# Optimization experiments

Hardware: AMD Instinct MI355X
Metric: run time of the kernel (lower is better)

The kernel has to match this reference:

```python
import jax, jax.numpy as jnp
import numpy as np

B, T, D, H = 1024, 128, 128, 8
HS = D // H  # 16, matches the hard-coded 16**-0.5 scale
EPS = 1e-5


def setup_inputs() -> dict:
    key = jax.random.key(0)
    ks = jax.random.split(key, 12)
    s = 0.02
    return {
        "x": jax.random.normal(ks[0], (B, T, D), jnp.float32),
        "Wq": jax.random.normal(ks[1], (H, D, HS), jnp.float32) * s,
        "Wk": jax.random.normal(ks[2], (H, D, HS), jnp.float32) * s,
        "Wv": jax.random.normal(ks[3], (H, D, HS), jnp.float32) * s,
        "Wo": jax.random.normal(ks[4], (D, D), jnp.float32) * s,
        "bo": jnp.zeros((D,), jnp.float32),
        "W1": jax.random.normal(ks[5], (D, 4 * D), jnp.float32) * s,
        "b1": jnp.zeros((4 * D,), jnp.float32),
        "W2": jax.random.normal(ks[6], (4 * D, D), jnp.float32) * s,
        "b2": jnp.zeros((D,), jnp.float32),
        "g1": jnp.ones((D,), jnp.float32),
        "be1": jnp.zeros((D,), jnp.float32),
        "g2": jnp.ones((D,), jnp.float32),
        "be2": jnp.zeros((D,), jnp.float32),
    }


def _layernorm(x, g, b):
    mu = jnp.mean(x, axis=-1, keepdims=True)
    var = jnp.mean(jnp.square(x - mu), axis=-1, keepdims=True)
    return (x - mu) * jax.lax.rsqrt(var + EPS) * g + b


def _block(x, Wq, Wk, Wv, Wo, bo, W1, b1, W2, b2, g1, be1, g2, be2):
    h = _layernorm(x, g1, be1)
    q = jnp.einsum('btd,hde->bhte', h, Wq)
    k = jnp.einsum('btd,hde->bhte', h, Wk)
    v = jnp.einsum('btd,hde->bhte', h, Wv)
    scores = jnp.einsum('bhte,bhse->bhts', q, k) * (16.0 ** -0.5)
    causal = jnp.tril(jnp.ones((T, T), bool))
    scores = jnp.where(causal, scores, -jnp.inf)
    wei = jax.nn.softmax(scores, axis=-1)  # dropout off (eval)
    o = jnp.einsum('bhts,bhse->bhte', wei, v)
    o = jnp.transpose(o, (0, 2, 1, 3)).reshape(x.shape[0], T, D)  # concat heads
    x = x + (o @ Wo + bo)
    h2 = _layernorm(x, g2, be2)
    ff = jax.nn.relu(h2 @ W1 + b1) @ W2 + b2
    return x + ff


def reference(x, Wq, Wk, Wv, Wo, bo, W1, b1, W2, b2, g1, be1, g2, be2):
    return _block(x, Wq, Wk, Wv, Wo, bo, W1, b1, W2, b2, g1, be1, g2, be2)
```

## Files before the change

### kernel.cpp

```cpp
#include <hip/hip_runtime.h>
#include <hip/hip_bf16.h>

typedef unsigned short u16;
typedef unsigned int u32;
typedef __bf16 bf16x8 __attribute__((ext_vector_type(8)));
typedef float f32x4 __attribute__((ext_vector_type(4)));

#define LDA 136

__device__ __forceinline__ u16 f2b(float f) {
  __bf16 b = (__bf16)f;
  return __builtin_bit_cast(u16, b);
}
__device__ __forceinline__ float b2f(u16 h) {
  u32 u = ((u32)h) << 16;
  return __builtin_bit_cast(float, u);
}
__device__ __forceinline__ u32 pk2(float lo, float hi) {
  return (u32)f2b(lo) | ((u32)f2b(hi) << 16);
}
__device__ __forceinline__ bf16x8 zero8() {
  union { int4 i; bf16x8 v; } u;
  u.i = make_int4(0, 0, 0, 0);
  return u.v;
}
__device__ __forceinline__ f32x4 mfma16(bf16x8 a, bf16x8 b, f32x4 c) {
  return __builtin_amdgcn_mfma_f32_16x16x32_bf16(a, b, c, 0, 0, 0);
}
__device__ __forceinline__ ushort4 pk4(float a, float b, float c, float d) {
  ushort4 r; r.x = f2b(a); r.y = f2b(b); r.z = f2b(c); r.w = f2b(d);
  return r;
}

__device__ __forceinline__ bf16x8 gatherB(const f32x4& ve, const f32x4& vo,
                                          bool odd_valid, float scale,
                                          int l15, int lg) {
  u32 pe0 = pk2(ve[0] * scale, ve[1] * scale);
  u32 pe1 = pk2(ve[2] * scale, ve[3] * scale);
  u32 po0 = 0, po1 = 0;
  if (odd_valid) {
    po0 = pk2(vo[0] * scale, vo[1] * scale);
    po1 = pk2(vo[2] * scale, vo[3] * scale);
  }
  int s0 = ((lg & 1) * 2) * 16 + l15;
  u32 a0 = __shfl(pe0, s0),      a1 = __shfl(pe1, s0);
  u32 a2 = __shfl(pe0, s0 + 16), a3 = __shfl(pe1, s0 + 16);
  u32 b0 = __shfl(po0, s0),      b1 = __shfl(po1, s0);
  u32 b2 = __shfl(po0, s0 + 16), b3 = __shfl(po1, s0 + 16);
  union { u32 u[4]; bf16x8 v; } fr;
  bool lo = (lg < 2);
  fr.u[0] = lo ? a0 : b0; fr.u[1] = lo ? a1 : b1;
  fr.u[2] = lo ? a2 : b2; fr.u[3] = lo ? a3 : b3;
  return fr.v;
}

__global__ void prep_kernel(const float* __restrict__ Wq, const float* __restrict__ Wk,
                            const float* __restrict__ Wv, const float* __restrict__ Wo,
                            const float* __restrict__ W1, const float* __restrict__ W2,
                            u16* __restrict__ o) {
  int i = blockIdx.x * 256 + threadIdx.x;
  if (i >= 196608) return;
  float v;
  if (i < 49152) {
    int which = i >> 14, j = i & 16383;
    int n = j >> 7, k = j & 127;
    const float* W = (which == 0) ? Wq : (which == 1) ? Wk : Wv;
    v = W[((n >> 4) * 128 + k) * 16 + (n & 15)];
  } else if (i < 65536) {
    int j = i - 49152;
    v = Wo[(j & 127) * 128 + (j >> 7)];
  } else if (i < 131072) {
    int j = i - 65536;
    v = W1[(j & 127) * 512 + (j >> 7)];
  } else {
    int j = i - 131072;
    int c = j & 127, r = (j >> 7) & 15, nt = (j >> 11) & 7, cc = j >> 14;
    v = W2[(cc * 128 + c) * 128 + nt * 16 + r];
  }
  o[i] = f2b(v);
}

__global__ void __launch_bounds__(512, 4)
tblock_kernel(const float* __restrict__ xg, const u16* __restrict__ wts,
              const float* __restrict__ bo, const float* __restrict__ b1,
              const float* __restrict__ b2, const float* __restrict__ g1,
              const float* __restrict__ be1, const float* __restrict__ g2,
              const float* __restrict__ be2, float* __restrict__ out) {
  extern __shared__ u16 sm[];
  u16* buf1 = sm;
  u16* buf2 = sm + 128 * LDA;

  const int tid  = threadIdx.x;
  const int w    = tid >> 6;
  const int lane = tid & 63;
  const int l15  = lane & 15;
  const int lg   = lane >> 4;

  const u16* WqT = wts;
  const u16* WkT = wts + 16384;
  const u16* WvT = wts + 32768;
  const u16* WoT = wts + 49152;
  const u16* W1T = wts + 65536;
  const u16* W2S = wts + 131072;

  const float* xp = xg + (size_t)blockIdx.x * 16384;
  float*       op = out + (size_t)blockIdx.x * 16384;

  const f32x4 zf4 = {0.f, 0.f, 0.f, 0.f};
  const bf16x8 zb8 = zero8();

  {
    const int t = w * 16 + l15;
    float v[8][4];
    #pragma unroll
    for (int nt = 0; nt < 8; ++nt) {
      float4 f = *(const float4*)(xp + t * 128 + nt * 16 + lg * 4);
      v[nt][0] = f.x; v[nt][1] = f.y; v[nt][2] = f.z; v[nt][3] = f.w;
    }
    float ps[8];
    #pragma unroll
    for (int nt = 0; nt < 8; ++nt)
      ps[nt] = (v[nt][0] + v[nt][1]) + (v[nt][2] + v[nt][3]);
    float s = ((ps[0] + ps[1]) + (ps[2] + ps[3])) +
              ((ps[4] + ps[5]) + (ps[6] + ps[7]));
    s += __shfl_xor(s, 16); s += __shfl_xor(s, 32);
    float mu = s * 0.0078125f;
    float pv[8];
    #pragma unroll
    for (int nt = 0; nt < 8; ++nt) {
      float d0 = v[nt][0] - mu, d1 = v[nt][1] - mu;
      float d2 = v[nt][2] - mu, d3 = v[nt][3] - mu;
      pv[nt] = (d0 * d0 + d1 * d1) + (d2 * d2 + d3 * d3);
    }
    float vv = ((pv[0] + pv[1]) + (pv[2] + pv[3])) +
               ((pv[4] + pv[5]) + (pv[6] + pv[7]));
    vv += __shfl_xor(vv, 16); vv += __shfl_xor(vv, 32);
    float rs = rsqrtf(vv * 0.0078125f + 1e-5f);
    #pragma unroll
    for (int nt = 0; nt < 8; ++nt) {
      float4 gv = *(const float4*)(g1 + nt * 16 + lg * 4);
      float4 bv = *(const float4*)(be1 + nt * 16 + lg * 4);
      *(ushort4*)(buf1 + t * LDA + nt * 16 + lg * 4) =
          pk4((v[nt][0] - mu) * rs * gv.x + bv.x, (v[nt][1] - mu) * rs * gv.y + bv.y,
              (v[nt][2] - mu) * rs * gv.z + bv.z, (v[nt][3] - mu) * rs * gv.w + bv.w);
    }
  }
  __syncthreads();

  bf16x8 av[4];
  {
    bf16x8 bw[4];
    #pragma unroll
    for (int kk = 0; kk < 4; ++kk)
      bw[kk] = *(const bf16x8*)(WvT + (w * 16 + l15) * 128 + kk * 32 + lg * 8);
    f32x4 vprev = zf4;
    #pragma unroll
    for (int mt = 0; mt < 8; ++mt) {
      f32x4 va = zf4;
      #pragma unroll
      for (int kk = 0; kk < 4; ++kk)
        va = mfma16(*(const bf16x8*)(buf1 + (mt * 16 + l15) * LDA + kk * 32 + lg * 8),
                    bw[kk], va);
      if (mt & 1) av[mt >> 1] = gatherB(vprev, va, true, 1.f, l15, lg);
      else        vprev = va;
    }
  }

  {
    bf16x8 bw[4];
    #pragma unroll
    for (int kk = 0; kk < 4; ++kk)
      bw[kk] = *(const bf16x8*)(WkT + (w * 16 + l15) * 128 + kk * 32 + lg * 8);
    #pragma unroll
    for (int mt = 0; mt < 8; ++mt) {
      f32x4 ka = zf4;
      #pragma unroll
      for (int kk = 0; kk < 4; ++kk)
        ka = mfma16(*(const bf16x8*)(buf1 + (mt * 16 + l15) * LDA + kk * 32 + lg * 8),
                    bw[kk], ka);
      #pragma unroll
      for (int rg = 0; rg < 4; ++rg)
        buf2[(mt * 16 + lg * 4 + rg) * LDA + w * 16 + l15] = f2b(ka[rg]);
    }
  }
  bf16x8 bk[8];
  #pragma unroll
  for (int st = 0; st < 8; ++st) {
    bk[st] = zb8;
    if (lg < 2)
      bk[st] = *(const bf16x8*)(buf2 + (st * 16 + l15) * LDA + w * 16 + lg * 8);
  }

  {
    bf16x8 bw[4];
    #pragma unroll
    for (int kk = 0; kk < 4; ++kk)
      bw[kk] = *(const bf16x8*)(WqT + (w * 16 + l15) * 128 + kk * 32 + lg * 8);
    #pragma unroll
    for (int mt = 0; mt < 8; ++mt) {
      f32x4 qa = zf4;
      #pragma unroll
      for (int kk = 0; kk < 4; ++kk)
        qa = mfma16(*(const bf16x8*)(buf1 + (mt * 16 + l15) * LDA + kk * 32 + lg * 8),
                    bw[kk], qa);
      #pragma unroll
      for (int rg = 0; rg < 4; ++rg)
        buf2[(mt * 16 + lg * 4 + rg) * LDA + w * 16 + l15] = f2b(qa[rg]);
    }
  }

  #pragma unroll 1
  for (int mt = 0; mt < 8; ++mt) {
    bf16x8 aq = zb8;
    if (lg < 2)
      aq = *(const bf16x8*)(buf2 + (mt * 16 + l15) * LDA + w * 16 + lg * 8);

    f32x4 sacc[8];
    #pragma unroll
    for (int st = 0; st < 8; ++st)
      sacc[st] = (st <= mt) ? mfma16(bk[st], aq, zf4) : zf4;

    float ps[8];
    #pragma unroll
    for (int st = 0; st < 8; ++st) {
      if (st <= mt) {
        #pragma unroll
        for (int rg = 0; rg < 4; ++rg) {
          float sv = sacc[st][rg] * 0.25f;
          bool ok = (st < mt) || ((lg * 4 + rg) <= l15);
          sv = ok ? sv : -1.0e30f;
          sacc[st][rg] = __expf(sv);
        }
        ps[st] = (sacc[st][0] + sacc[st][1]) + (sacc[st][2] + sacc[st][3]);
      } else {
        ps[st] = 0.f;
      }
    }
    float sum = ((ps[0] + ps[1]) + (ps[2] + ps[3])) +
                ((ps[4] + ps[5]) + (ps[6] + ps[7]));
    sum += __shfl_xor(sum, 16);
    sum += __shfl_xor(sum, 32);
    float inv = 1.f / sum;

    f32x4 oa = zf4;
    #pragma unroll
    for (int kk = 0; kk < 4; ++kk) if (kk <= (mt >> 1)) {
      bf16x8 fr = gatherB(sacc[2 * kk], sacc[2 * kk + 1], (2 * kk + 1) <= mt, inv, l15, lg);
      oa = mfma16(av[kk], fr, oa);
    }
    *(ushort4*)(buf2 + (mt * 16 + l15) * LDA + w * 16 + lg * 4) =
        pk4(oa[0], oa[1], oa[2], oa[3]);
  }
  __syncthreads();

  f32x4 oacc2[8];
  {
    bf16x8 bw[4];
    #pragma unroll
    for (int kk = 0; kk < 4; ++kk)
      bw[kk] = *(const bf16x8*)(WoT + (w * 16 + l15) * 128 + kk * 32 + lg * 8);
    float bov = bo[w * 16 + l15];
    float b2v = b2[w * 16 + l15];
    #pragma unroll
    for (int mt = 0; mt < 8; ++mt) {
      float xrl[4];
      #pragma unroll
      for (int rg = 0; rg < 4; ++rg)
        xrl[rg] = xp[(mt * 16 + lg * 4 + rg) * 128 + w * 16 + l15];
      f32x4 acc = zf4;
      #pragma unroll
      for (int kk = 0; kk < 4; ++kk)
        acc = mfma16(*(const bf16x8*)(buf2 + (mt * 16 + l15) * LDA + kk * 32 + lg * 8),
                     bw[kk], acc);
      #pragma unroll
      for (int rg = 0; rg < 4; ++rg) {
        float x1v = acc[rg] + bov + xrl[rg];
        buf1[(mt * 16 + lg * 4 + rg) * LDA + w * 16 + l15] = f2b(x1v);
        oacc2[mt][rg] = x1v + b2v;
      }
    }
  }
  __syncthreads();

  {
    const int t = w * 16 + l15;
    float v[8][4];
    #pragma unroll
    for (int nt = 0; nt < 8; ++nt) {
      ushort4 u = *(const ushort4*)(buf1 + t * LDA + nt * 16 + lg * 4);
      v[nt][0] = b2f(u.x); v[nt][1] = b2f(u.y); v[nt][2] = b2f(u.z); v[nt][3] = b2f(u.w);
    }
    float ps[8];
    #pragma unroll
    for (int nt = 0; nt < 8; ++nt)
      ps[nt] = (v[nt][0] + v[nt][1]) + (v[nt][2] + v[nt][3]);
    float s = ((ps[0] + ps[1]) + (ps[2] + ps[3])) +
              ((ps[4] + ps[5]) + (ps[6] + ps[7]));
    s += __shfl_xor(s, 16); s += __shfl_xor(s, 32);
    float mu = s * 0.0078125f;
    float pv[8];
    #pragma unroll
    for (int nt = 0; nt < 8; ++nt) {
      float d0 = v[nt][0] - mu, d1 = v[nt][1] - mu;
      float d2 = v[nt][2] - mu, d3 = v[nt][3] - mu;
      pv[nt] = (d0 * d0 + d1 * d1) + (d2 * d2 + d3 * d3);
    }
    float vv = ((pv[0] + pv[1]) + (pv[2] + pv[3])) +
               ((pv[4] + pv[5]) + (pv[6] + pv[7]));
    vv += __shfl_xor(vv, 16); vv += __shfl_xor(vv, 32);
    float rs = rsqrtf(vv * 0.0078125f + 1e-5f);
    #pragma unroll
    for (int nt = 0; nt < 8; ++nt) {
      float4 gv = *(const float4*)(g2 + nt * 16 + lg * 4);
      float4 bv = *(const float4*)(be2 + nt * 16 + lg * 4);
      *(ushort4*)(buf1 + t * LDA + nt * 16 + lg * 4) =
          pk4((v[nt][0] - mu) * rs * gv.x + bv.x, (v[nt][1] - mu) * rs * gv.y + bv.y,
              (v[nt][2] - mu) * rs * gv.z + bv.z, (v[nt][3] - mu) * rs * gv.w + bv.w);
    }
  }
  __syncthreads();

  #pragma unroll 1
  for (int cc = 0; cc < 4; ++cc) {
    {
      bf16x8 bw1[4];
      #pragma unroll
      for (int kk = 0; kk < 4; ++kk)
        bw1[kk] = *(const bf16x8*)(W1T + (cc * 128 + w * 16 + l15) * 128 + kk * 32 + lg * 8);
      float b1v = b1[cc * 128 + w * 16 + l15];
      #pragma unroll
      for (int mt = 0; mt < 8; ++mt) {
        f32x4 facc = zf4;
        #pragma unroll
        for (int kk = 0; kk < 4; ++kk)
          facc = mfma16(*(const bf16x8*)(buf1 + (mt * 16 + l15) * LDA + kk * 32 + lg * 8),
                        bw1[kk], facc);
        #pragma unroll
        for (int rg = 0; rg < 4; ++rg)
          buf2[(mt * 16 + lg * 4 + rg) * LDA + w * 16 + l15] =
              f2b(fmaxf(facc[rg] + b1v, 0.f));
      }
    }
    __syncthreads();

    {
      bf16x8 bw2[4];
      #pragma unroll
      for (int kk = 0; kk < 4; ++kk)
        bw2[kk] = *(const bf16x8*)(W2S + ((cc * 8 + w) * 16 + l15) * 128 + kk * 32 + lg * 8);
      #pragma unroll
      for (int mt = 0; mt < 8; ++mt)
        #pragma unroll
        for (int kk = 0; kk < 4; ++kk)
          oacc2[mt] = mfma16(*(const bf16x8*)(buf2 + (mt * 16 + l15) * LDA + kk * 32 + lg * 8),
                             bw2[kk], oacc2[mt]);
    }
    if (cc < 3) __syncthreads();
  }

  #pragma unroll
  for (int mt = 0; mt < 8; ++mt)
    #pragma unroll
    for (int rg = 0; rg < 4; ++rg)
      op[(mt * 16 + lg * 4 + rg) * 128 + w * 16 + l15] = oacc2[mt][rg];
}

extern "C" void kernel_launch(void* const* d_in, const int* in_sizes, int n_in,
                              void* d_out, int out_size, void* d_ws, size_t ws_size,
                              hipStream_t stream) {
  const float* x   = (const float*)d_in[0];
  const float* Wq  = (const float*)d_in[1];
  const float* Wk  = (const float*)d_in[2];
  const float* Wv  = (const float*)d_in[3];
  const float* Wo  = (const float*)d_in[4];
  const float* bo  = (const float*)d_in[5];
  const float* W1  = (const float*)d_in[6];
  const float* b1  = (const float*)d_in[7];
  const float* W2  = (const float*)d_in[8];
  const float* b2  = (const float*)d_in[9];
  const float* g1  = (const float*)d_in[10];
  const float* be1 = (const float*)d_in[11];
  const float* g2  = (const float*)d_in[12];
  const float* be2 = (const float*)d_in[13];
  u16* wts = (u16*)d_ws;

  prep_kernel<<<768, 256, 0, stream>>>(Wq, Wk, Wv, Wo, W1, W2, wts);

  const int smem_bytes = 2 * 128 * LDA * 2;
  hipFuncSetAttribute(reinterpret_cast<const void*>(tblock_kernel),
                      hipFuncAttributeMaxDynamicSharedMemorySize, smem_bytes);
  tblock_kernel<<<1024, 512, smem_bytes, stream>>>(x, wts, bo, b1, b2, g1, be1, g2,
                                                   be2, (float*)d_out);
}
```

Baseline: 148.4 us.

## Restructure attention and MLP to keep K, Q and FFN intermediates in registers

Keeps K and Q projections in registers as packed bf16 and builds the K operand by lane shuffles instead of staging through a second LDS buffer. Softmax is fused with the PV product, with normalization applied afterwards. The output projection, LayerNorm2 and MLP are re-partitioned so each wave owns 16 token rows. The MLP hidden activations stay in registers via shuffles, which removes the LDS round-trips and the block-level barriers inside the FFN loop. LDS use is halved, which may allow higher occupancy, but every wave now reads all W1/W2/Wo weights from global memory, raising global and cache traffic.

After: 384.9 us. 159% more time.

```diff
diff --git a/kernel.cpp b/kernel.cpp
--- a/kernel.cpp
+++ b/kernel.cpp
@@ -51,6 +51,19 @@
   bool lo = (lg < 2);
   fr.u[0] = lo ? a0 : b0; fr.u[1] = lo ? a1 : b1;
   fr.u[2] = lo ? a2 : b2; fr.u[3] = lo ? a3 : b3;
+  return fr.v;
+}
+
+__device__ __forceinline__ bf16x8 buildK(u32 k0, u32 k1, int l15, int lg) {
+  int lgc = lg & 1;
+  u32 r0 = __shfl(k0, (2 * lgc + 0) * 16 + l15);
+  u32 r1 = __shfl(k1, (2 * lgc + 0) * 16 + l15);
+  u32 r2 = __shfl(k0, (2 * lgc + 1) * 16 + l15);
+  u32 r3 = __shfl(k1, (2 * lgc + 1) * 16 + l15);
+  union { u32 u[4]; bf16x8 v; } fr;
+  bool lo = (lg < 2);
+  fr.u[0] = lo ? r0 : 0; fr.u[1] = lo ? r1 : 0;
+  fr.u[2] = lo ? r2 : 0; fr.u[3] = lo ? r3 : 0;
   return fr.v;
 }
 
@@ -74,8 +87,8 @@
     v = W1[(j & 127) * 512 + (j >> 7)];
   } else {
     int j = i - 131072;
-    int c = j & 127, r = (j >> 7) & 15, nt = (j >> 11) & 7, cc = j >> 14;
-    v = W2[(cc * 128 + c) * 128 + nt * 16 + r];
+    int c = j >> 9, n = j & 511;
+    v = W2[n * 128 + c];
   }
   o[i] = f2b(v);
 }
@@ -88,7 +101,6 @@
               const float* __restrict__ be2, float* __restrict__ out) {
   extern __shared__ u16 sm[];
   u16* buf1 = sm;
-  u16* buf2 = sm + 128 * LDA;
 
   const int tid  = threadIdx.x;
   const int w    = tid >> 6;
@@ -96,12 +108,12 @@
   const int l15  = lane & 15;
   const int lg   = lane >> 4;
 
-  const u16* WqT = wts;
-  const u16* WkT = wts + 16384;
-  const u16* WvT = wts + 32768;
-  const u16* WoT = wts + 49152;
-  const u16* W1T = wts + 65536;
-  const u16* W2S = wts + 131072;
+  const u16* WqT  = wts;
+  const u16* WkT  = wts + 16384;
+  const u16* WvT  = wts + 32768;
+  const u16* WoT  = wts + 49152;
+  const u16* W1T  = wts + 65536;
+  const u16* W2T2 = wts + 131072;
 
   const float* xp = xg + (size_t)blockIdx.x * 16384;
   float*       op = out + (size_t)blockIdx.x * 16384;
@@ -166,31 +178,26 @@
     }
   }
 
+  u32 kp[8][2];
   {
     bf16x8 bw[4];
     #pragma unroll
     for (int kk = 0; kk < 4; ++kk)
       bw[kk] = *(const bf16x8*)(WkT + (w * 16 + l15) * 128 + kk * 32 + lg * 8);
     #pragma unroll
-    for (int mt = 0; mt < 8; ++mt) {
+    for (int st = 0; st < 8; ++st) {
       f32x4 ka = zf4;
       #pragma unroll
       for (int kk = 0; kk < 4; ++kk)
-        ka = mfma16(*(const bf16x8*)(buf1 + (mt * 16 + l15) * LDA + kk * 32 + lg * 8),
-                    bw[kk], ka);
-      #pragma unroll
-      for (int rg = 0; rg < 4; ++rg)
-        buf2[(mt * 16 + lg * 4 + rg) * LDA + w * 16 + l15] = f2b(ka[rg]);
-    }
-  }
-  bf16x8 bk[8];
-  #pragma unroll
-  for (int st = 0; st < 8; ++st) {
-    bk[st] = zb8;
-    if (lg < 2)
-      bk[st] = *(const bf16x8*)(buf2 + (st * 16 + l15) * LDA + w * 16 + lg * 8);
-  }
-
+        ka = mfma16(bw[kk],
+                    *(const bf16x8*)(buf1 + (st * 16 + l15) * LDA + kk * 32 + lg * 8),
+                    ka);
+      kp[st][0] = pk2(ka[0], ka[1]);
+      kp[st][1] = pk2(ka[2], ka[3]);
+    }
+  }
+
+  u32 qp[8][2];
   {
     bf16x8 bw[4];
     #pragma unroll
@@ -201,168 +208,159 @@
       f32x4 qa = zf4;
       #pragma unroll
       for (int kk = 0; kk < 4; ++kk)
-        qa = mfma16(*(const bf16x8*)(buf1 + (mt * 16 + l15) * LDA + kk * 32 + lg * 8),
-                    bw[kk], qa);
-      #pragma unroll
-      for (int rg = 0; rg < 4; ++rg)
-        buf2[(mt * 16 + lg * 4 + rg) * LDA + w * 16 + l15] = f2b(qa[rg]);
-    }
+        qa = mfma16(bw[kk],
+                    *(const bf16x8*)(buf1 + (mt * 16 + l15) * LDA + kk * 32 + lg * 8),
+                    qa);
+      qp[mt][0] = pk2(qa[0], qa[1]);
+      qp[mt][1] = pk2(qa[2], qa[3]);
+    }
+  }
+  __syncthreads();
+
+  #pragma unroll
+  for (int mt = 0; mt < 8; ++mt) {
+    union { u32 u[2]; ushort4 s; } uq;
+    uq.u[0] = qp[mt][0]; uq.u[1] = qp[mt][1];
+    *(ushort4*)(buf1 + (mt * 16 + l15) * LDA + w * 16 + lg * 4) = uq.s;
   }
 
   #pragma unroll 1
   for (int mt = 0; mt < 8; ++mt) {
     bf16x8 aq = zb8;
     if (lg < 2)
-      aq = *(const bf16x8*)(buf2 + (mt * 16 + l15) * LDA + w * 16 + lg * 8);
-
-    f32x4 sacc[8];
-    #pragma unroll
-    for (int st = 0; st < 8; ++st)
-      sacc[st] = (st <= mt) ? mfma16(bk[st], aq, zf4) : zf4;
-
-    float ps[8];
-    #pragma unroll
-    for (int st = 0; st < 8; ++st) {
-      if (st <= mt) {
-        #pragma unroll
-        for (int rg = 0; rg < 4; ++rg) {
-          float sv = sacc[st][rg] * 0.25f;
-          bool ok = (st < mt) || ((lg * 4 + rg) <= l15);
-          sv = ok ? sv : -1.0e30f;
-          sacc[st][rg] = __expf(sv);
-        }
-        ps[st] = (sacc[st][0] + sacc[st][1]) + (sacc[st][2] + sacc[st][3]);
-      } else {
-        ps[st] = 0.f;
+      aq = *(const bf16x8*)(buf1 + (mt * 16 + l15) * LDA + w * 16 + lg * 8);
+
+    float sum = 0.f;
+    f32x4 oa = zf4;
+    #pragma unroll
+    for (int kk = 0; kk < 4; ++kk) if (kk <= (mt >> 1)) {
+      const int s0i = 2 * kk, s1i = 2 * kk + 1;
+      f32x4 e0 = mfma16(buildK(kp[s0i][0], kp[s0i][1], l15, lg), aq, zf4);
+      f32x4 e1 = zf4;
+      bool odd = (s1i <= mt);
+      if (odd)
+        e1 = mfma16(buildK(kp[s1i][0], kp[s1i][1], l15, lg), aq, zf4);
+      #pragma unroll
+      for (int rg = 0; rg < 4; ++rg) {
+        float sv0 = e0[rg] * 0.25f;
+        bool ok0 = (s0i < mt) || ((lg * 4 + rg) <= l15);
+        e0[rg] = __expf(ok0 ? sv0 : -1.0e30f);
+        float sv1 = e1[rg] * 0.25f;
+        bool ok1 = (s1i < mt) || ((lg * 4 + rg) <= l15);
+        e1[rg] = odd ? __expf(ok1 ? sv1 : -1.0e30f) : 0.f;
       }
-    }
-    float sum = ((ps[0] + ps[1]) + (ps[2] + ps[3])) +
-                ((ps[4] + ps[5]) + (ps[6] + ps[7]));
+      sum += ((e0[0] + e0[1]) + (e0[2] + e0[3])) +
+             ((e1[0] + e1[1]) + (e1[2] + e1[3]));
+      bf16x8 fr = gatherB(e0, e1, odd, 1.f, l15, lg);
+      oa = mfma16(av[kk], fr, oa);
+    }
     sum += __shfl_xor(sum, 16);
     sum += __shfl_xor(sum, 32);
     float inv = 1.f / sum;
-
-    f32x4 oa = zf4;
-    #pragma unroll
-    for (int kk = 0; kk < 4; ++kk) if (kk <= (mt >> 1)) {
-      bf16x8 fr = gatherB(sacc[2 * kk], sacc[2 * kk + 1], (2 * kk + 1) <= mt, inv, l15, lg);
-      oa = mfma16(av[kk], fr, oa);
-    }
-    *(ushort4*)(buf2 + (mt * 16 + l15) * LDA + w * 16 + lg * 4) =
-        pk4(oa[0], oa[1], oa[2], oa[3]);
+    *(ushort4*)(buf1 + (mt * 16 + l15) * LDA + w * 16 + lg * 4) =
+        pk4(oa[0] * inv, oa[1] * inv, oa[2] * inv, oa[3] * inv);
   }
   __syncthreads();
 
-  f32x4 oacc2[8];
-  {
-    bf16x8 bw[4];
-    #pragma unroll
-    for (int kk = 0; kk < 4; ++kk)
-      bw[kk] = *(const bf16x8*)(WoT + (w * 16 + l15) * 128 + kk * 32 + lg * 8);
-    float bov = bo[w * 16 + l15];
-    float b2v = b2[w * 16 + l15];
-    #pragma unroll
-    for (int mt = 0; mt < 8; ++mt) {
-      float xrl[4];
+  f32x4 x1r[8];
+  {
+    bf16x8 ofr[4];
+    #pragma unroll
+    for (int kk = 0; kk < 4; ++kk)
+      ofr[kk] = *(const bf16x8*)(buf1 + (w * 16 + l15) * LDA + kk * 32 + lg * 8);
+    #pragma unroll
+    for (int nt = 0; nt < 8; ++nt) {
+      f32x4 acc = zf4;
+      #pragma unroll
+      for (int kk = 0; kk < 4; ++kk)
+        acc = mfma16(ofr[kk],
+                     *(const bf16x8*)(WoT + (nt * 16 + l15) * 128 + kk * 32 + lg * 8),
+                     acc);
+      float bov = bo[nt * 16 + l15];
       #pragma unroll
       for (int rg = 0; rg < 4; ++rg)
-        xrl[rg] = xp[(mt * 16 + lg * 4 + rg) * 128 + w * 16 + l15];
-      f32x4 acc = zf4;
-      #pragma unroll
-      for (int kk = 0; kk < 4; ++kk)
-        acc = mfma16(*(const bf16x8*)(buf2 + (mt * 16 + l15) * LDA + kk * 32 + lg * 8),
-                     bw[kk], acc);
-      #pragma unroll
-      for (int rg = 0; rg < 4; ++rg) {
-        float x1v = acc[rg] + bov + xrl[rg];
-        buf1[(mt * 16 + lg * 4 + rg) * LDA + w * 16 + l15] = f2b(x1v);
-        oacc2[mt][rg] = x1v + b2v;
+        x1r[nt][rg] = acc[rg] + bov + xp[(w * 16 + lg * 4 + rg) * 128 + nt * 16 + l15];
+    }
+  }
+
+  {
+    float ps[8];
+    #pragma unroll
+    for (int nt = 0; nt < 8; ++nt)
+      ps[nt] = (x1r[nt][0] + x1r[nt][1]) + (x1r[nt][2] + x1r[nt][3]);
+    #pragma unroll
+    for (int rg = 0; rg < 4; ++rg) {
+      float s = ((x1r[0][rg] + x1r[1][rg]) + (x1r[2][rg] + x1r[3][rg])) +
+                ((x1r[4][rg] + x1r[5][rg]) + (x1r[6][rg] + x1r[7][rg]));
+      s += __shfl_xor(s, 1); s += __shfl_xor(s, 2);
+      s += __shfl_xor(s, 4); s += __shfl_xor(s, 8);
+      float mu = s * 0.0078125f;
+      float vv = 0.f;
+      {
+        float q[8];
+        #pragma unroll
+        for (int nt = 0; nt < 8; ++nt) { float d = x1r[nt][rg] - mu; q[nt] = d * d; }
+        vv = ((q[0] + q[1]) + (q[2] + q[3])) + ((q[4] + q[5]) + (q[6] + q[7]));
       }
-    }
-  }
-  __syncthreads();
-
-  {
-    const int t = w * 16 + l15;
-    float v[8][4];
-    #pragma unroll
-    for (int nt = 0; nt < 8; ++nt) {
-      ushort4 u = *(const ushort4*)(buf1 + t * LDA + nt * 16 + lg * 4);
-      v[nt][0] = b2f(u.x); v[nt][1] = b2f(u.y); v[nt][2] = b2f(u.z); v[nt][3] = b2f(u.w);
-    }
-    float ps[8];
-    #pragma unroll
-    for (int nt = 0; nt < 8; ++nt)
-      ps[nt] = (v[nt][0] + v[nt][1]) + (v[nt][2] + v[nt][3]);
-    float s = ((ps[0] + ps[1]) + (ps[2] + ps[3])) +
-              ((ps[4] + ps[5]) + (ps[6] + ps[7]));
-    s += __shfl_xor(s, 16); s += __shfl_xor(s, 32);
-    float mu = s * 0.0078125f;
-    float pv[8];
-    #pragma unroll
-    for (int nt = 0; nt < 8; ++nt) {
-      float d0 = v[nt][0] - mu, d1 = v[nt][1] - mu;
-      float d2 = v[nt][2] - mu, d3 = v[nt][3] - mu;
-      pv[nt] = (d0 * d0 + d1 * d1) + (d2 * d2 + d3 * d3);
-    }
-    float vv = ((pv[0] + pv[1]) + (pv[2] + pv[3])) +
-               ((pv[4] + pv[5]) + (pv[6] + pv[7]));
-    vv += __shfl_xor(vv, 16); vv += __shfl_xor(vv, 32);
-    float rs = rsqrtf(vv * 0.0078125f + 1e-5f);
-    #pragma unroll
-    for (int nt = 0; nt < 8; ++nt) {
-      float4 gv = *(const float4*)(g2 + nt * 16 + lg * 4);
-      float4 bv = *(const float4*)(be2 + nt * 16 + lg * 4);
-      *(ushort4*)(buf1 + t * LDA + nt * 16 + lg * 4) =
-          pk4((v[nt][0] - mu) * rs * gv.x + bv.x, (v[nt][1] - mu) * rs * gv.y + bv.y,
-              (v[nt][2] - mu) * rs * gv.z + bv.z, (v[nt][3] - mu) * rs * gv.w + bv.w);
-    }
-  }
-  __syncthreads();
-
-  #pragma unroll 1
-  for (int cc = 0; cc < 4; ++cc) {
-    {
-      bf16x8 bw1[4];
-      #pragma unroll
-      for (int kk = 0; kk < 4; ++kk)
-        bw1[kk] = *(const bf16x8*)(W1T + (cc * 128 + w * 16 + l15) * 128 + kk * 32 + lg * 8);
-      float b1v = b1[cc * 128 + w * 16 + l15];
-      #pragma unroll
-      for (int mt = 0; mt < 8; ++mt) {
-        f32x4 facc = zf4;
+      vv += __shfl_xor(vv, 1); vv += __shfl_xor(vv, 2);
+      vv += __shfl_xor(vv, 4); vv += __shfl_xor(vv, 8);
+      float rs = rsqrtf(vv * 0.0078125f + 1e-5f);
+      #pragma unroll
+      for (int nt = 0; nt < 8; ++nt) {
+        int col = nt * 16 + l15;
+        float h2 = (x1r[nt][rg] - mu) * rs * g2[col] + be2[col];
+        buf1[(w * 16 + lg * 4 + rg) * LDA + col] = f2b(h2);
+      }
+    }
+    (void)ps;
+  }
+
+  {
+    bf16x8 hf2[4];
+    #pragma unroll
+    for (int kk = 0; kk < 4; ++kk)
+      hf2[kk] = *(const bf16x8*)(buf1 + (w * 16 + l15) * LDA + kk * 32 + lg * 8);
+
+    #pragma unroll 1
+    for (int m = 0; m < 16; ++m) {
+      f32x4 f0 = zf4, f1 = zf4;
+      {
+        bf16x8 w1a[4];
         #pragma unroll
         for (int kk = 0; kk < 4; ++kk)
-          facc = mfma16(*(const bf16x8*)(buf1 + (mt * 16 + l15) * LDA + kk * 32 + lg * 8),
-                        bw1[kk], facc);
-        #pragma unroll
-        for (int rg = 0; rg < 4; ++rg)
-          buf2[(mt * 16 + lg * 4 + rg) * LDA + w * 16 + l15] =
-              f2b(fmaxf(facc[rg] + b1v, 0.f));
+          w1a[kk] = *(const bf16x8*)(W1T + (m * 32 + l15) * 128 + kk * 32 + lg * 8);
+        #pragma unroll
+        for (int kk = 0; kk < 4; ++kk)
+          f0 = mfma16(w1a[kk], hf2[kk], f0);
+        #pragma unroll
+        for (int kk = 0; kk < 4; ++kk)
+          w1a[kk] = *(const bf16x8*)(W1T + (m * 32 + 16 + l15) * 128 + kk * 32 + lg * 8);
+        #pragma unroll
+        for (int kk = 0; kk < 4; ++kk)
+          f1 = mfma16(w1a[kk], hf2[kk], f1);
       }
-    }
-    __syncthreads();
-
-    {
-      bf16x8 bw2[4];
-      #pragma unroll
-      for (int kk = 0; kk < 4; ++kk)
-        bw2[kk] = *(const bf16x8*)(W2S + ((cc * 8 + w) * 16 + l15) * 128 + kk * 32 + lg * 8);
-      #pragma unroll
-      for (int mt = 0; mt < 8; ++mt)
-        #pragma unroll
-        for (int kk = 0; kk < 4; ++kk)
-          oacc2[mt] = mfma16(*(const bf16x8*)(buf2 + (mt * 16 + l15) * LDA + kk * 32 + lg * 8),
-                             bw2[kk], oacc2[mt]);
-    }
-    if (cc < 3) __syncthreads();
+      float4 b1v0 = *(const float4*)(b1 + m * 32 + lg * 4);
+      float4 b1v1 = *(const float4*)(b1 + m * 32 + 16 + lg * 4);
+      f0[0] = fmaxf(f0[0] + b1v0.x, 0.f); f0[1] = fmaxf(f0[1] + b1v0.y, 0.f);
+      f0[2] = fmaxf(f0[2] + b1v0.z, 0.f); f0[3] = fmaxf(f0[3] + b1v0.w, 0.f);
+      f1[0] = fmaxf(f1[0] + b1v1.x, 0.f); f1[1] = fmaxf(f1[1] + b1v1.y, 0.f);
+      f1[2] = fmaxf(f1[2] + b1v1.z, 0.f); f1[3] = fmaxf(f1[3] + b1v1.w, 0.f);
+      bf16x8 rf = gatherB(f0, f1, true, 1.f, l15, lg);
+      #pragma unroll
+      for (int nt = 0; nt < 8; ++nt)
+        x1r[nt] = mfma16(rf,
+                         *(const bf16x8*)(W2T2 + (nt * 16 + l15) * 512 + m * 32 + lg * 8),
+                         x1r[nt]);
+    }
   }
 
   #pragma unroll
-  for (int mt = 0; mt < 8; ++mt)
+  for (int nt = 0; nt < 8; ++nt) {
+    float b2v = b2[nt * 16 + l15];
     #pragma unroll
     for (int rg = 0; rg < 4; ++rg)
-      op[(mt * 16 + lg * 4 + rg) * 128 + w * 16 + l15] = oacc2[mt][rg];
+      op[(w * 16 + lg * 4 + rg) * 128 + nt * 16 + l15] = x1r[nt][rg] + b2v;
+  }
 }
 
 extern "C" void kernel_launch(void* const* d_in, const int* in_sizes, int n_in,
@@ -386,7 +384,7 @@
 
   prep_kernel<<<768, 256, 0, stream>>>(Wq, Wk, Wv, Wo, W1, W2, wts);
 
-  const int smem_bytes = 2 * 128 * LDA * 2;
+  const int smem_bytes = 128 * LDA * 2;
   hipFuncSetAttribute(reinterpret_cast<const void*>(tblock_kernel),
                       hipFuncAttributeMaxDynamicSharedMemorySize, smem_bytes);
   tblock_kernel<<<1024, 512, smem_bytes, stream>>>(x, wts, bo, b1, b2, g1, be1, g2,
```
